# Optimization experiments

Hardware: AMD Instinct MI355X
Metric: run time of the kernel (lower is better)

The kernel has to match this reference:

```python
import jax, jax.numpy as jnp
from jax import lax
import numpy as np

NS, NC = 12, 4            # n_state, n_ctrl
NSC = NS + NC             # tau = [x; u]
T, B = 50, 2048
U_LO, U_HI = -1.0, 1.0
LQR_ITERS = 3             # qp_iter-style outer LQR iterations
N_LS = 5                  # max_linesearch_iter
LS_DECAY = 0.5            # linesearch_decay


def setup_inputs() -> dict:
    key = jax.random.key(0)
    k0, k1, k2, k3, k4 = jax.random.split(key, 5)
    x0 = jax.random.normal(k0, (B, NS), jnp.float32)
    # PD quadratic cost: C = 0.1 * A A^T + I  (symmetric positive definite)
    A = jax.random.normal(k1, (T, B, NSC, NSC), jnp.float32) * (1.0 / np.sqrt(NSC))
    C = 0.1 * jnp.einsum('tbik,tbjk->tbij', A, A) + jnp.eye(NSC, dtype=jnp.float32)
    c = jax.random.normal(k2, (T, B, NSC), jnp.float32)
    # Near-identity stable linear dynamics x' = F [x;u] + f
    F = 0.02 * jax.random.normal(k3, (T, B, NS, NSC), jnp.float32)
    eye_pad = jnp.concatenate([0.98 * jnp.eye(NS, dtype=jnp.float32),
                               jnp.zeros((NS, NC), jnp.float32)], axis=-1)
    F = F + eye_pad
    f = 0.01 * jax.random.normal(k4, (T, B, NS), jnp.float32)
    return {'x0': x0, 'C': C, 'c': c, 'F': F, 'f': f}


def _riccati(C, c, F, f):
    """Backward Riccati recursion. Returns feedback gains K [T,B,NC,NS], k [T,B,NC]."""
    def step(carry, inp):
        V, v = carry                      # V: [B,NS,NS], v: [B,NS]
        Ct, ct, Ft, ft = inp
        FtV = jnp.einsum('bki,bkl->bil', Ft, V)          # F^T V: [B,NSC,NS]
        Q = Ct + jnp.einsum('bil,blj->bij', FtV, Ft)     # [B,NSC,NSC]
        q = ct + jnp.einsum('bki,bk->bi', Ft,
                            jnp.einsum('bij,bj->bi', V, ft) + v)
        Qxx, Qxu = Q[:, :NS, :NS], Q[:, :NS, NS:]
        Qux, Quu = Q[:, NS:, :NS], Q[:, NS:, NS:]
        qx, qu = q[:, :NS], q[:, NS:]
        rhs = jnp.concatenate([Qux, qu[:, :, None]], axis=-1)  # [B,NC,NS+1]
        sol = jnp.linalg.solve(Quu, rhs)
        K = -sol[:, :, :NS]               # [B,NC,NS]
        kk = -sol[:, :, NS]               # [B,NC]
        QxuK = jnp.einsum('bij,bjk->bik', Qxu, K)
        V_new = Qxx + QxuK + QxuK.transpose(0, 2, 1) \
            + jnp.einsum('bji,bjl,blk->bik', K, Quu, K)
        V_new = 0.5 * (V_new + V_new.transpose(0, 2, 1))
        v_new = qx + jnp.einsum('bij,bj->bi', Qxu, kk) \
            + jnp.einsum('bji,bj->bi', K, qu + jnp.einsum('bij,bj->bi', Quu, kk))
        return (V_new, v_new), (K, kk)

    Vz = jnp.zeros((C.shape[1], NS, NS), C.dtype)
    vz = jnp.zeros((C.shape[1], NS), C.dtype)
    _, (K, kk) = lax.scan(step, (Vz, vz), (C, c, F, f), reverse=True)
    return K, kk


def _rollout(alpha, x0, u_nom, K, kk, C, c, F, f):
    """Forward pass with box-clamped controls and line-search blending."""
    def step(carry, inp):
        x, cost = carry
        Ct, ct, Ft, ft, Kt, kt, unomt = inp
        u_lqr = jnp.einsum('bij,bj->bi', Kt, x) + kt
        u = jnp.clip((1.0 - alpha) * unomt + alpha * u_lqr, U_LO, U_HI)
        tau = jnp.concatenate([x, u], axis=-1)            # [B,NSC]
        cost = cost + 0.5 * jnp.einsum('bi,bij,bj->b', tau, Ct, tau) \
            + jnp.einsum('bi,bi->b', ct, tau)
        x_next = jnp.einsum('bij,bj->bi', Ft, tau) + ft
        return (x_next, cost), tau

    init = (x0, jnp.zeros(x0.shape[0], x0.dtype))
    (_, cost), taus = lax.scan(step, init, (C, c, F, f, K, kk, u_nom))
    return cost, taus  # cost [B], taus [T,B,NSC]


def reference(x0, C, c, F, f):
    alphas = LS_DECAY ** jnp.arange(N_LS, dtype=C.dtype)  # [N_LS]
    u_nom = jnp.zeros((T, x0.shape[0], NC), x0.dtype)
    taus = None
    for _ in range(LQR_ITERS):
        K, kk = _riccati(C, c, F, f)
        costs, taus_all = jax.vmap(
            lambda a: _rollout(a, x0, u_nom, K, kk, C, c, F, f))(alphas)
        # costs: [N_LS,B]; taus_all: [N_LS,T,B,NSC]. Pick best alpha per batch elem.
        best = jnp.argmin(costs, axis=0)                  # [B]
        taus = jnp.take_along_axis(taus_all,
                                   best[None, None, :, None], axis=0)[0]
        u_nom = taus[:, :, NS:]
    return taus  # [T, B, NSC] optimized trajectory [x; u]
```

## Files before the change

kernel.cpp:

```cpp
#include <hip/hip_runtime.h>
#include <math.h>

#define T_   50
#define B_   2048
#define NS_  12
#define NC_  4
#define NSC_ 16
#define LDC  20
#define TAUS_STRIDE 808

__device__ __forceinline__ float dot4f(const float4 a, const float4 b) {
    return a.x*b.x + a.y*b.y + a.z*b.z + a.w*b.w;
}
__device__ __forceinline__ void axpy4(float4& acc, float s, const float4 v) {
    acc.x += s*v.x; acc.y += s*v.y; acc.z += s*v.z; acc.w += s*v.w;
}

__device__ __forceinline__ void wsync() {
    __builtin_amdgcn_wave_barrier();
    __builtin_amdgcn_s_waitcnt(0xC07F);
    __builtin_amdgcn_wave_barrier();
}

struct RicPref { float4 rC, rAux; };

__device__ __forceinline__ RicPref ric_load(
    const float* Cg, const float* cg, const float* Fg, const float* fg,
    int t, int b, int lane)
{
    RicPref p;
    const size_t base = (size_t)t * B_ + b;
    p.rC = ((const float4*)(Cg + base*256))[lane];
    if (lane < 48)      p.rAux = ((const float4*)(Fg + base*192))[lane];
    else if (lane < 52) p.rAux = ((const float4*)(cg + base*16))[lane-48];
    else if (lane < 55) p.rAux = ((const float4*)(fg + base*12))[lane-52];
    return p;
}

__global__ __launch_bounds__(64) void riccati_kernel(
    const float* __restrict__ Cg, const float* __restrict__ cg,
    const float* __restrict__ Fg, const float* __restrict__ fg,
    float* __restrict__ Kk)
{
    const int b    = blockIdx.x;
    const int lane = threadIdx.x;

    __shared__ __align__(16) float sV[144];
    __shared__ __align__(16) float sv[12];
    __shared__ __align__(16) float sF[12*LDC];
    __shared__ __align__(16) float sC[16*LDC];
    __shared__ __align__(16) float sc[16];
    __shared__ __align__(16) float sf[12];
    __shared__ __align__(16) float sP[12*LDC];
    __shared__ __align__(16) float sQ[16*LDC];
    __shared__ __align__(16) float sq[16];
    __shared__ __align__(16) float stmp[12];
    __shared__ __align__(16) float sK[48];
    __shared__ __align__(16) float skk[4];
    __shared__ __align__(16) float sM[144];

    for (int i = lane; i < 144; i += 64) sV[i] = 0.f;
    if (lane < 12) sv[lane] = 0.f;

    RicPref cur = ric_load(Cg, cg, Fg, fg, T_-1, b, lane);
    wsync();

    for (int t = T_ - 1; t >= 0; --t) {
        const size_t base = (size_t)t * B_ + b;

        wsync();
        {
            const int row = lane >> 2, ch = (lane & 3) << 2;
            *(float4*)(sC + row*LDC + ch) = cur.rC;
            if (lane < 48)      *(float4*)(sF + row*LDC + ch) = cur.rAux;
            else if (lane < 52) ((float4*)sc)[lane-48] = cur.rAux;
            else if (lane < 55) ((float4*)sf)[lane-52] = cur.rAux;
        }
        RicPref nxt = ric_load(Cg, cg, Fg, fg, (t > 0) ? t-1 : 0, b, lane);
        wsync();

        if (lane < 48) {
            const int k = lane >> 2, jc = (lane & 3) << 2;
            float4 acc = make_float4(0.f,0.f,0.f,0.f);
            #pragma unroll
            for (int l = 0; l < 12; ++l) {
                axpy4(acc, sV[k*12 + l], *(const float4*)(sF + l*LDC + jc));
            }
            *(float4*)(sP + k*LDC + jc) = acc;
        } else if (lane < 60) {
            const int k = lane - 48;
            float acc = sv[k];
            #pragma unroll
            for (int l = 0; l < 12; ++l) acc += sV[k*12 + l] * sf[l];
            stmp[k] = acc;
        }
        wsync();

        {
            const int i = lane >> 2, jc = (lane & 3) << 2;
            float4 acc = *(const float4*)(sC + i*LDC + jc);
            #pragma unroll
            for (int k = 0; k < 12; ++k) {
                axpy4(acc, sF[k*LDC + i], *(const float4*)(sP + k*LDC + jc));
            }
            *(float4*)(sQ + i*LDC + jc) = acc;
        }
        if (lane < 16) {
            float acc = sc[lane];
            #pragma unroll
            for (int k = 0; k < 12; ++k) acc += sF[k*LDC + lane] * stmp[k];
            sq[lane] = acc;
        }
        wsync();

        {
            const float* Qu = sQ + 12*LDC + 12;
            const float a00=Qu[0],      a01=Qu[1],      a02=Qu[2],      a03=Qu[3];
            const float a11=Qu[LDC+1],  a12=Qu[LDC+2],  a13=Qu[LDC+3];
            const float a22=Qu[2*LDC+2],a23=Qu[2*LDC+3],a33=Qu[3*LDC+3];
            const float l00 = sqrtf(a00), i00 = 1.f/l00;
            const float l10 = a01*i00, l20 = a02*i00, l30 = a03*i00;
            const float l11 = sqrtf(a11 - l10*l10), i11 = 1.f/l11;
            const float l21 = (a12 - l20*l10)*i11;
            const float l31 = (a13 - l30*l10)*i11;
            const float l22 = sqrtf(a22 - l20*l20 - l21*l21), i22 = 1.f/l22;
            const float l32 = (a23 - l30*l20 - l31*l21)*i22;
            const float l33 = sqrtf(a33 - l30*l30 - l31*l31 - l32*l32), i33 = 1.f/l33;
            if (lane < 13) {
                float r0, r1, r2, r3;
                if (lane < 12) {
                    r0 = sQ[12*LDC + lane]; r1 = sQ[13*LDC + lane];
                    r2 = sQ[14*LDC + lane]; r3 = sQ[15*LDC + lane];
                } else {
                    r0 = sq[12]; r1 = sq[13]; r2 = sq[14]; r3 = sq[15];
                }
                const float y0 = r0*i00;
                const float y1 = (r1 - l10*y0)*i11;
                const float y2 = (r2 - l20*y0 - l21*y1)*i22;
                const float y3 = (r3 - l30*y0 - l31*y1 - l32*y2)*i33;
                const float z3 = y3*i33;
                const float z2 = (y2 - l32*z3)*i22;
                const float z1 = (y1 - l21*z2 - l31*z3)*i11;
                const float z0 = (y0 - l10*z1 - l20*z2 - l30*z3)*i00;
                if (lane < 12) {
                    sK[0*12+lane] = -z0; sK[1*12+lane] = -z1;
                    sK[2*12+lane] = -z2; sK[3*12+lane] = -z3;
                } else {
                    skk[0] = -z0; skk[1] = -z1; skk[2] = -z2; skk[3] = -z3;
                }
            }
        }
        wsync();

        if (lane < 52) {
            (Kk + base*52)[lane] = (lane < 48) ? sK[lane] : skk[lane-48];
        }
        if (lane < 36) {
            const int i = lane / 3, jc = (lane % 3) << 2;
            float4 acc = make_float4(0.f,0.f,0.f,0.f);
            #pragma unroll
            for (int m = 0; m < 4; ++m) {
                axpy4(acc, sK[m*12 + i], *(const float4*)(sQ + (12+m)*LDC + jc));
            }
            *(float4*)(sM + i*12 + jc) = acc;
        } else if (lane < 48) {
            const int i = lane - 36;
            float acc = sq[i];
            #pragma unroll
            for (int m = 0; m < 4; ++m) acc += sQ[i*LDC + 12 + m] * skk[m];
            sv[i] = acc;
        }
        wsync();

        if (lane < 36) {
            const int i = lane / 3, jc = (lane % 3) << 2;
            const float4 q  = *(const float4*)(sQ + i*LDC + jc);
            const float4 m1 = *(const float4*)(sM + i*12 + jc);
            const float t0 = sM[(jc+0)*12 + i];
            const float t1 = sM[(jc+1)*12 + i];
            const float t2 = sM[(jc+2)*12 + i];
            const float t3 = sM[(jc+3)*12 + i];
            float4 r;
            r.x = q.x + 0.5f*(m1.x + t0);
            r.y = q.y + 0.5f*(m1.y + t1);
            r.z = q.z + 0.5f*(m1.z + t2);
            r.w = q.w + 0.5f*(m1.w + t3);
            *(float4*)(sV + i*12 + jc) = r;
        }
        cur = nxt;
    }
}

struct RollPref { float4 rC, rAux, rcf; };

__device__ __forceinline__ RollPref roll_load(
    const float* Cg, const float* cg, const float* Fg, const float* fg,
    const float* Kk, int t, int b, int lane)
{
    RollPref p;
    const size_t base = (size_t)t * B_ + b;
    p.rC = ((const float4*)(Cg + base*256))[lane];
    if (lane < 48)      p.rAux = ((const float4*)(Fg + base*192))[lane];
    else if (lane < 61) p.rAux = ((const float4*)(Kk + base*52))[lane-48];
    if (lane < 4)       p.rcf = ((const float4*)(cg + base*16))[lane];
    else if (lane < 7)  p.rcf = ((const float4*)(fg + base*12))[lane-4];
    return p;
}

__global__ __launch_bounds__(64) void rollout_kernel(
    const float* __restrict__ x0g, const float* __restrict__ Cg,
    const float* __restrict__ cg,  const float* __restrict__ Fg,
    const float* __restrict__ fg,  const float* __restrict__ Kk,
    float* __restrict__ outg)
{
    const int b    = blockIdx.x;
    const int lane = threadIdx.x;

    __shared__ __align__(16) float staus[5*TAUS_STRIDE];
    __shared__ __align__(16) float sunom[T_*NC_];
    __shared__ __align__(16) float sx[5*12];
    __shared__ __align__(16) float sx0[12];
    __shared__ __align__(16) float sC[16*LDC];
    __shared__ __align__(16) float sF[12*LDC];
    __shared__ __align__(16) float sKk[56];
    __shared__ __align__(16) float sc[16];
    __shared__ __align__(16) float sf[12];
    __shared__ float scost[5];
    __shared__ int   sbest;

    for (int i = lane; i < T_*NC_; i += 64) sunom[i] = 0.f;
    if (lane < 3) ((float4*)sx0)[lane] = ((const float4*)(x0g + b*12))[lane];

    RollPref cur = roll_load(Cg, cg, Fg, fg, Kk, 0, b, lane);
    wsync();

    for (int iter = 0; iter < 3; ++iter) {
        if (lane < 60) sx[lane] = sx0[lane % 12];
        float ca = 0.f;
        float cb = 0.f;
        wsync();

        for (int t = 0; t < T_; ++t) {
            wsync();
            {
                const int row = lane >> 2, ch = (lane & 3) << 2;
                *(float4*)(sC + row*LDC + ch) = cur.rC;
                if (lane < 48)      *(float4*)(sF + row*LDC + ch) = cur.rAux;
                else if (lane < 61) ((float4*)sKk)[lane-48] = cur.rAux;
                if (lane < 4)       ((float4*)sc)[lane]   = cur.rcf;
                else if (lane < 7)  ((float4*)sf)[lane-4] = cur.rcf;
            }
            RollPref nxt = roll_load(Cg, cg, Fg, fg, Kk,
                                     (t+1 < T_) ? t+1 : 0, b, lane);
            wsync();

            if (lane < 20) {
                const int a = lane >> 2, i = lane & 3;
                const float* Kr = sKk + i*12;
                const float* xa = sx  + a*12;
                float ulqr = dot4f(*(const float4*)(Kr  ), *(const float4*)(xa  ))
                           + dot4f(*(const float4*)(Kr+4), *(const float4*)(xa+4))
                           + dot4f(*(const float4*)(Kr+8), *(const float4*)(xa+8))
                           + sKk[48 + i];
                const float al = ldexpf(1.0f, -a);
                float u = (1.f - al) * sunom[t*4 + i] + al * ulqr;
                u = fminf(1.f, fmaxf(-1.f, u));
                staus[a*TAUS_STRIDE + t*16 + 12 + i] = u;
            } else if (lane >= 32 && lane < 47) {
                const int idx = lane - 32;
                const int a = idx / 3, ch = (idx % 3) << 2;
                *(float4*)(staus + a*TAUS_STRIDE + t*16 + ch) =
                    *(const float4*)(sx + a*12 + ch);
            }
            wsync();

            {
                const int a = lane >> 4, i = lane & 15;
                const float* tau = staus + a*TAUS_STRIDE + t*16;
                const float* Cr  = sC + i*LDC;
                float acc = 0.f;
                #pragma unroll
                for (int chv = 0; chv < 4; ++chv) {
                    acc += dot4f(*(const float4*)(Cr + 4*chv),
                                 *(const float4*)(tau + 4*chv));
                }
                ca += (0.5f*acc + sc[i]) * tau[i];
            }
            if (lane < 16) {
                const int i = lane;
                const float* tau = staus + 4*TAUS_STRIDE + t*16;
                const float* Cr  = sC + i*LDC;
                float acc = 0.f;
                #pragma unroll
                for (int chv = 0; chv < 4; ++chv) {
                    acc += dot4f(*(const float4*)(Cr + 4*chv),
                                 *(const float4*)(tau + 4*chv));
                }
                cb += (0.5f*acc + sc[i]) * tau[i];
            }

            if (lane < 60) {
                const int a = lane / 12, i = lane - a*12;
                const float* tau = staus + a*TAUS_STRIDE + t*16;
                const float* Fr  = sF + i*LDC;
                float acc = sf[i];
                #pragma unroll
                for (int chv = 0; chv < 4; ++chv) {
                    acc += dot4f(*(const float4*)(Fr + 4*chv),
                                 *(const float4*)(tau + 4*chv));
                }
                sx[a*12 + i] = acc;
            }
            cur = nxt;
        }

        #pragma unroll
        for (int off = 1; off < 16; off <<= 1) {
            ca += __shfl_xor(ca, off, 16);
            cb += __shfl_xor(cb, off, 16);
        }
        if ((lane & 15) == 0) scost[lane >> 4] = ca;
        if (lane == 0) scost[4] = cb;
        wsync();
        if (lane == 0) {
            int bi = 0; float bc = scost[0];
            #pragma unroll
            for (int a = 1; a < 5; ++a) {
                if (scost[a] < bc) { bc = scost[a]; bi = a; }
            }
            sbest = bi;
        }
        wsync();
        const int best = sbest;

        for (int idx = lane; idx < T_*NC_; idx += 64) {
            const int tt = idx >> 2, i = idx & 3;
            sunom[idx] = staus[best*TAUS_STRIDE + tt*16 + 12 + i];
        }
        if (iter == 2) {
            for (int idx = lane; idx < T_*NSC_; idx += 64) {
                const int tt = idx >> 4, j = idx & 15;
                outg[((size_t)tt*B_ + b)*16 + j] = staus[best*TAUS_STRIDE + tt*16 + j];
            }
        }
        wsync();
    }
}

extern "C" void kernel_launch(void* const* d_in, const int* in_sizes, int n_in,
                              void* d_out, int out_size, void* d_ws, size_t ws_size,
                              hipStream_t stream) {
    const float* x0 = (const float*)d_in[0];
    const float* C  = (const float*)d_in[1];
    const float* c  = (const float*)d_in[2];
    const float* F  = (const float*)d_in[3];
    const float* f  = (const float*)d_in[4];
    float* out = (float*)d_out;
    float* Kk  = (float*)d_ws;

    riccati_kernel<<<B_, 64, 0, stream>>>(C, c, F, f, Kk);
    rollout_kernel<<<B_, 64, 0, stream>>>(x0, C, c, F, f, Kk, out);
}
```

Baseline: 427.8 us.

## Keep per-lane cost/dynamics rows in registers and restructure rollout lane mapping

The rollout kernel is reorganized so each lane owns one (alpha, state) pair and holds its rows of C, F, K and the matching c/f entries in registers, loaded directly from global memory. This drops the per-timestep staging of C/F/K into shared memory and one barrier per step. The riccati kernel keeps C in registers, reads V rows as float4 and folds the small vector products into the matrix lanes. In exchange there is more register pressure and redundant global loads, since five alpha groups read the same rows, and the final cost reduction now goes through shared memory.

```diff
diff --git a/kernel.cpp b/kernel.cpp
--- a/kernel.cpp
+++ b/kernel.cpp
@@ -7,7 +7,7 @@
 #define NC_  4
 #define NSC_ 16
 #define LDC  20
-#define TAUS_STRIDE 808
+#define AST  808
 
 __device__ __forceinline__ float dot4f(const float4 a, const float4 b) {
     return a.x*b.x + a.y*b.y + a.z*b.z + a.w*b.w;
@@ -48,7 +48,6 @@
     __shared__ __align__(16) float sV[144];
     __shared__ __align__(16) float sv[12];
     __shared__ __align__(16) float sF[12*LDC];
-    __shared__ __align__(16) float sC[16*LDC];
     __shared__ __align__(16) float sc[16];
     __shared__ __align__(16) float sf[12];
     __shared__ __align__(16) float sP[12*LDC];
@@ -69,9 +68,9 @@
         const size_t base = (size_t)t * B_ + b;
 
         wsync();
+        const float4 rCq = cur.rC;
         {
             const int row = lane >> 2, ch = (lane & 3) << 2;
-            *(float4*)(sC + row*LDC + ch) = cur.rC;
             if (lane < 48)      *(float4*)(sF + row*LDC + ch) = cur.rAux;
             else if (lane < 52) ((float4*)sc)[lane-48] = cur.rAux;
             else if (lane < 55) ((float4*)sf)[lane-52] = cur.rAux;
@@ -81,35 +80,42 @@
 
         if (lane < 48) {
             const int k = lane >> 2, jc = (lane & 3) << 2;
+            const float4 v0 = *(const float4*)(sV + k*12);
+            const float4 v1 = *(const float4*)(sV + k*12 + 4);
+            const float4 v2 = *(const float4*)(sV + k*12 + 8);
+            const float vk[12] = {v0.x,v0.y,v0.z,v0.w, v1.x,v1.y,v1.z,v1.w,
+                                  v2.x,v2.y,v2.z,v2.w};
             float4 acc = make_float4(0.f,0.f,0.f,0.f);
             #pragma unroll
             for (int l = 0; l < 12; ++l) {
-                axpy4(acc, sV[k*12 + l], *(const float4*)(sF + l*LDC + jc));
+                axpy4(acc, vk[l], *(const float4*)(sF + l*LDC + jc));
             }
             *(float4*)(sP + k*LDC + jc) = acc;
-        } else if (lane < 60) {
-            const int k = lane - 48;
-            float acc = sv[k];
-            #pragma unroll
-            for (int l = 0; l < 12; ++l) acc += sV[k*12 + l] * sf[l];
-            stmp[k] = acc;
+            if (jc == 0) {
+                float accT = sv[k];
+                #pragma unroll
+                for (int l = 0; l < 12; ++l) accT += vk[l] * sf[l];
+                stmp[k] = accT;
+            }
         }
         wsync();
 
         {
             const int i = lane >> 2, jc = (lane & 3) << 2;
-            float4 acc = *(const float4*)(sC + i*LDC + jc);
+            float4 acc = rCq;
+            float fcol[12];
             #pragma unroll
             for (int k = 0; k < 12; ++k) {
-                axpy4(acc, sF[k*LDC + i], *(const float4*)(sP + k*LDC + jc));
+                fcol[k] = sF[k*LDC + i];
+                axpy4(acc, fcol[k], *(const float4*)(sP + k*LDC + jc));
             }
             *(float4*)(sQ + i*LDC + jc) = acc;
-        }
-        if (lane < 16) {
-            float acc = sc[lane];
-            #pragma unroll
-            for (int k = 0; k < 12; ++k) acc += sF[k*LDC + lane] * stmp[k];
-            sq[lane] = acc;
+            if (jc == 0) {
+                float accq = sc[i];
+                #pragma unroll
+                for (int k = 0; k < 12; ++k) accq += fcol[k] * stmp[k];
+                sq[i] = accq;
+            }
         }
         wsync();
 
@@ -191,19 +197,34 @@
     }
 }
 
-struct RollPref { float4 rC, rAux, rcf; };
-
-__device__ __forceinline__ RollPref roll_load(
+struct Pref {
+    float4 C0, C1, C2, C3;
+    float4 D0, D1, D2, D3;
+    float4 F0, F1, F2, F3;
+    float4 K0, K1, K2;
+    float  kk, ci, c2i, fi;
+};
+
+__device__ __forceinline__ Pref pload(
     const float* Cg, const float* cg, const float* Fg, const float* fg,
-    const float* Kk, int t, int b, int lane)
+    const float* Kk, int t, int b, int i, bool ul)
 {
-    RollPref p;
+    Pref p;
     const size_t base = (size_t)t * B_ + b;
-    p.rC = ((const float4*)(Cg + base*256))[lane];
-    if (lane < 48)      p.rAux = ((const float4*)(Fg + base*192))[lane];
-    else if (lane < 61) p.rAux = ((const float4*)(Kk + base*52))[lane-48];
-    if (lane < 4)       p.rcf = ((const float4*)(cg + base*16))[lane];
-    else if (lane < 7)  p.rcf = ((const float4*)(fg + base*12))[lane-4];
+    const float4* Cr = (const float4*)(Cg + base*256 + i*16);
+    p.C0 = Cr[0]; p.C1 = Cr[1]; p.C2 = Cr[2]; p.C3 = Cr[3];
+    const float4* Fr = (const float4*)(Fg + base*192 + i*16);
+    p.F0 = Fr[0]; p.F1 = Fr[1]; p.F2 = Fr[2]; p.F3 = Fr[3];
+    p.ci = cg[base*16 + i];
+    p.fi = fg[base*12 + i];
+    if (ul) {
+        const float4* Dr = (const float4*)(Cg + base*256 + (12+i)*16);
+        p.D0 = Dr[0]; p.D1 = Dr[1]; p.D2 = Dr[2]; p.D3 = Dr[3];
+        const float4* Kr = (const float4*)(Kk + base*52 + i*12);
+        p.K0 = Kr[0]; p.K1 = Kr[1]; p.K2 = Kr[2];
+        p.kk  = Kk[base*52 + 48 + i];
+        p.c2i = cg[base*16 + 12 + i];
+    }
     return p;
 }
 
@@ -215,133 +236,93 @@
 {
     const int b    = blockIdx.x;
     const int lane = threadIdx.x;
-
-    __shared__ __align__(16) float staus[5*TAUS_STRIDE];
+    int a = lane / 12;
+    int i = lane - a*12;
+    const bool act = (lane < 60);
+    if (!act) { a = 4; i = lane - 52; }
+    const bool ulane = act && (i < 4);
+    const float alpha = ldexpf(1.0f, -a);
+
+    __shared__ __align__(16) float staus[5*AST];
     __shared__ __align__(16) float sunom[T_*NC_];
-    __shared__ __align__(16) float sx[5*12];
-    __shared__ __align__(16) float sx0[12];
-    __shared__ __align__(16) float sC[16*LDC];
-    __shared__ __align__(16) float sF[12*LDC];
-    __shared__ __align__(16) float sKk[56];
-    __shared__ __align__(16) float sc[16];
-    __shared__ __align__(16) float sf[12];
-    __shared__ float scost[5];
-    __shared__ int   sbest;
-
-    for (int i = lane; i < T_*NC_; i += 64) sunom[i] = 0.f;
-    if (lane < 3) ((float4*)sx0)[lane] = ((const float4*)(x0g + b*12))[lane];
-
-    RollPref cur = roll_load(Cg, cg, Fg, fg, Kk, 0, b, lane);
+    __shared__ __align__(16) float spart[64];
+    __shared__ __align__(16) float scost[8];
+    __shared__ int sbest;
+
+    const float x0v = x0g[b*12 + i];
+    if (lane < 50) *(float4*)(sunom + lane*4) = make_float4(0.f,0.f,0.f,0.f);
+
+    Pref cur = pload(Cg, cg, Fg, fg, Kk, 0, b, i, ulane);
     wsync();
 
     for (int iter = 0; iter < 3; ++iter) {
-        if (lane < 60) sx[lane] = sx0[lane % 12];
-        float ca = 0.f;
-        float cb = 0.f;
-        wsync();
+        float xv   = x0v;
+        float cacc = 0.f;
 
         for (int t = 0; t < T_; ++t) {
+            float* tb = staus + a*AST + t*16;
+            if (act) tb[i] = xv;
+            Pref nxt = pload(Cg, cg, Fg, fg, Kk, (t+1 < T_) ? t+1 : 0, b, i, ulane);
             wsync();
-            {
-                const int row = lane >> 2, ch = (lane & 3) << 2;
-                *(float4*)(sC + row*LDC + ch) = cur.rC;
-                if (lane < 48)      *(float4*)(sF + row*LDC + ch) = cur.rAux;
-                else if (lane < 61) ((float4*)sKk)[lane-48] = cur.rAux;
-                if (lane < 4)       ((float4*)sc)[lane]   = cur.rcf;
-                else if (lane < 7)  ((float4*)sf)[lane-4] = cur.rcf;
-            }
-            RollPref nxt = roll_load(Cg, cg, Fg, fg, Kk,
-                                     (t+1 < T_) ? t+1 : 0, b, lane);
+            const float4 xA = *(const float4*)(tb);
+            const float4 xB = *(const float4*)(tb + 4);
+            const float4 xC = *(const float4*)(tb + 8);
+            if (ulane) {
+                const float ulqr = dot4f(cur.K0, xA) + dot4f(cur.K1, xB)
+                                 + dot4f(cur.K2, xC) + cur.kk;
+                const float un = sunom[t*4 + i];
+                float u = (1.f - alpha)*un + alpha*ulqr;
+                u = fminf(1.f, fmaxf(-1.f, u));
+                tb[12 + i] = u;
+            }
             wsync();
-
-            if (lane < 20) {
-                const int a = lane >> 2, i = lane & 3;
-                const float* Kr = sKk + i*12;
-                const float* xa = sx  + a*12;
-                float ulqr = dot4f(*(const float4*)(Kr  ), *(const float4*)(xa  ))
-                           + dot4f(*(const float4*)(Kr+4), *(const float4*)(xa+4))
-                           + dot4f(*(const float4*)(Kr+8), *(const float4*)(xa+8))
-                           + sKk[48 + i];
-                const float al = ldexpf(1.0f, -a);
-                float u = (1.f - al) * sunom[t*4 + i] + al * ulqr;
-                u = fminf(1.f, fmaxf(-1.f, u));
-                staus[a*TAUS_STRIDE + t*16 + 12 + i] = u;
-            } else if (lane >= 32 && lane < 47) {
-                const int idx = lane - 32;
-                const int a = idx / 3, ch = (idx % 3) << 2;
-                *(float4*)(staus + a*TAUS_STRIDE + t*16 + ch) =
-                    *(const float4*)(sx + a*12 + ch);
-            }
-            wsync();
-
-            {
-                const int a = lane >> 4, i = lane & 15;
-                const float* tau = staus + a*TAUS_STRIDE + t*16;
-                const float* Cr  = sC + i*LDC;
-                float acc = 0.f;
-                #pragma unroll
-                for (int chv = 0; chv < 4; ++chv) {
-                    acc += dot4f(*(const float4*)(Cr + 4*chv),
-                                 *(const float4*)(tau + 4*chv));
-                }
-                ca += (0.5f*acc + sc[i]) * tau[i];
-            }
-            if (lane < 16) {
-                const int i = lane;
-                const float* tau = staus + 4*TAUS_STRIDE + t*16;
-                const float* Cr  = sC + i*LDC;
-                float acc = 0.f;
-                #pragma unroll
-                for (int chv = 0; chv < 4; ++chv) {
-                    acc += dot4f(*(const float4*)(Cr + 4*chv),
-                                 *(const float4*)(tau + 4*chv));
-                }
-                cb += (0.5f*acc + sc[i]) * tau[i];
-            }
-
-            if (lane < 60) {
-                const int a = lane / 12, i = lane - a*12;
-                const float* tau = staus + a*TAUS_STRIDE + t*16;
-                const float* Fr  = sF + i*LDC;
-                float acc = sf[i];
-                #pragma unroll
-                for (int chv = 0; chv < 4; ++chv) {
-                    acc += dot4f(*(const float4*)(Fr + 4*chv),
-                                 *(const float4*)(tau + 4*chv));
-                }
-                sx[a*12 + i] = acc;
-            }
+            const float4 uA = *(const float4*)(tb + 12);
+            const float cc = dot4f(cur.C0, xA) + dot4f(cur.C1, xB)
+                           + dot4f(cur.C2, xC) + dot4f(cur.C3, uA);
+            cacc += (0.5f*cc + cur.ci) * xv;
+            if (ulane) {
+                const float cc2 = dot4f(cur.D0, xA) + dot4f(cur.D1, xB)
+                                + dot4f(cur.D2, xC) + dot4f(cur.D3, uA);
+                const float uval = (i == 0) ? uA.x : (i == 1) ? uA.y
+                                 : (i == 2) ? uA.z : uA.w;
+                cacc += (0.5f*cc2 + cur.c2i) * uval;
+            }
+            xv = dot4f(cur.F0, xA) + dot4f(cur.F1, xB)
+               + dot4f(cur.F2, xC) + dot4f(cur.F3, uA) + cur.fi;
             cur = nxt;
         }
 
-        #pragma unroll
-        for (int off = 1; off < 16; off <<= 1) {
-            ca += __shfl_xor(ca, off, 16);
-            cb += __shfl_xor(cb, off, 16);
-        }
-        if ((lane & 15) == 0) scost[lane >> 4] = ca;
-        if (lane == 0) scost[4] = cb;
+        spart[lane] = act ? cacc : 0.f;
+        wsync();
+        if (lane < 5) {
+            float s = 0.f;
+            #pragma unroll
+            for (int j = 0; j < 12; ++j) s += spart[lane*12 + j];
+            scost[lane] = s;
+        }
         wsync();
         if (lane == 0) {
             int bi = 0; float bc = scost[0];
             #pragma unroll
-            for (int a = 1; a < 5; ++a) {
-                if (scost[a] < bc) { bc = scost[a]; bi = a; }
+            for (int aa = 1; aa < 5; ++aa) {
+                if (scost[aa] < bc) { bc = scost[aa]; bi = aa; }
             }
             sbest = bi;
         }
         wsync();
         const int best = sbest;
 
-        for (int idx = lane; idx < T_*NC_; idx += 64) {
-            const int tt = idx >> 2, i = idx & 3;
-            sunom[idx] = staus[best*TAUS_STRIDE + tt*16 + 12 + i];
-        }
-        if (iter == 2) {
-            for (int idx = lane; idx < T_*NSC_; idx += 64) {
-                const int tt = idx >> 4, j = idx & 15;
-                outg[((size_t)tt*B_ + b)*16 + j] = staus[best*TAUS_STRIDE + tt*16 + j];
-            }
+        if (lane < 50) {
+            const float4 uu = *(const float4*)(staus + best*AST + lane*16 + 12);
+            *(float4*)(sunom + lane*4) = uu;
+        }
+        if (iter == 2 && lane < 50) {
+            const float* src = staus + best*AST + lane*16;
+            float* dst = outg + ((size_t)lane*B_ + b)*16;
+            *(float4*)(dst)      = *(const float4*)(src);
+            *(float4*)(dst + 4)  = *(const float4*)(src + 4);
+            *(float4*)(dst + 8)  = *(const float4*)(src + 8);
+            *(float4*)(dst + 12) = *(const float4*)(src + 12);
         }
         wsync();
     }
```

After: 477.5 us. 1.12x slower.
